# Optimization experiments

Measured on AMD Instinct MI355X. Metric: run time of the kernel, lower is better.

The kernel has to match this reference:

```python
import jax, jax.numpy as jnp
import numpy as np

B, N = 128, 1369
DINO, CLIP, H = 384, 512, 8
D = CLIP // H  # head_dim = 64
EPS = 1e-5


def setup_inputs() -> dict:
    key = jax.random.key(0)
    ks = jax.random.split(key, 8)
    s_clip = 1.0 / np.sqrt(CLIP)
    s_dino = 1.0 / np.sqrt(DINO)
    return {
        "dino_features": jax.random.normal(ks[0], (B, N, DINO), jnp.float32),
        "clip_features": jax.random.normal(ks[1], (B, CLIP), jnp.float32),
        "Wq": jax.random.uniform(ks[2], (CLIP, CLIP), jnp.float32, -s_clip, s_clip),
        "bq": jnp.zeros((CLIP,), jnp.float32),
        "Wk": jax.random.uniform(ks[3], (DINO, CLIP), jnp.float32, -s_dino, s_dino),
        "bk": jnp.zeros((CLIP,), jnp.float32),
        "Wv": jax.random.uniform(ks[4], (DINO, CLIP), jnp.float32, -s_dino, s_dino),
        "bv": jnp.zeros((CLIP,), jnp.float32),
        "temperature": jnp.ones((1,), jnp.float32),
        "ln_gamma": jnp.ones((CLIP,), jnp.float32),
        "ln_beta": jnp.zeros((CLIP,), jnp.float32),
    }


def reference(dino_features, clip_features, Wq, bq, Wk, bk, Wv, bv,
              temperature, ln_gamma, ln_beta):
    # Q: (B, H, D) -- single query token from CLIP
    Q = (clip_features @ Wq + bq).reshape(B, H, D)
    # K, V: (B, N, H, D)
    K = (dino_features @ Wk + bk).reshape(B, N, H, D)
    V = (dino_features @ Wv + bv).reshape(B, N, H, D)
    scale = jnp.sqrt(jnp.float32(D)) * temperature[0]
    # attention logits over patches: (B, H, N)
    logits = jnp.einsum("bhd,bnhd->bhn", Q, K) / scale
    attn = jax.nn.softmax(logits, axis=-1)  # dropout is identity in eval mode
    out = jnp.einsum("bhn,bnhd->bhd", attn, V).reshape(B, CLIP)
    # LayerNorm over last dim
    mu = out.mean(axis=-1, keepdims=True)
    var = out.var(axis=-1, keepdims=True)
    return (out - mu) * jax.lax.rsqrt(var + EPS) * ln_gamma + ln_beta
```

## Files before the change

kernel.cpp:

```cpp
#include <hip/hip_runtime.h>
#include <math.h>

#define B_    128
#define N_    1369
#define DINO_ 384
#define CLIP_ 512
#define H_    8
#define CHUNKS 6
#define CH     229
#define SMP    52

__device__ __forceinline__ float wave_sum(float v) {
  v += __shfl_xor(v, 1);  v += __shfl_xor(v, 2);  v += __shfl_xor(v, 4);
  v += __shfl_xor(v, 8);  v += __shfl_xor(v, 16); v += __shfl_xor(v, 32);
  return v;
}

__global__ __launch_bounds__(256) void kq(const float* __restrict__ clip,
                                          const float* __restrict__ Wq,
                                          const float* __restrict__ bq,
                                          float* __restrict__ Q) {
  const int b = blockIdx.x;
  const int c = blockIdx.y * 256 + threadIdx.x;
  __shared__ float cl[CLIP_];
  cl[threadIdx.x] = clip[b * CLIP_ + threadIdx.x];
  cl[threadIdx.x + 256] = clip[b * CLIP_ + threadIdx.x + 256];
  __syncthreads();
  float acc = bq[c];
  #pragma unroll 8
  for (int j = 0; j < CLIP_; ++j) acc += cl[j] * Wq[j * CLIP_ + c];
  Q[b * CLIP_ + c] = acc;
}

__global__ __launch_bounds__(256) void kqk(const float* __restrict__ Wk,
                                           const float* __restrict__ Q,
                                           const float* __restrict__ temp,
                                           float* __restrict__ qkout) {
  const int b = blockIdx.x;
  const int e = blockIdx.y * 256 + threadIdx.x;
  __shared__ float qs[CLIP_];
  qs[threadIdx.x] = Q[b * CLIP_ + threadIdx.x];
  qs[threadIdx.x + 256] = Q[b * CLIP_ + threadIdx.x + 256];
  __syncthreads();
  const int h = e / DINO_;
  const int j = e - h * DINO_;
  const float rs = 1.0f / (8.0f * temp[0]);
  const float* wrow = Wk + (size_t)j * CLIP_ + h * 64;
  const float* qrow = qs + h * 64;
  float a0 = 0.f, a1 = 0.f, a2 = 0.f, a3 = 0.f;
  #pragma unroll
  for (int d = 0; d < 64; d += 4) {
    const float4 wv = *(const float4*)(wrow + d);
    const float4 qv = *(const float4*)(qrow + d);
    a0 += wv.x * qv.x;  a1 += wv.y * qv.y;
    a2 += wv.z * qv.z;  a3 += wv.w * qv.w;
  }
  qkout[(size_t)b * 3072 + e] = ((a0 + a1) + (a2 + a3)) * rs;
}

__global__ __launch_bounds__(256, 3) void kmain(const float* __restrict__ dino,
                                                const float* __restrict__ qk,
                                                float* __restrict__ ps,
                                                float* __restrict__ pl) {
  const int blk = blockIdx.x;
  const int b = blk / CHUNKS;
  const int c = blk - b * CHUNKS;
  const int n0 = c * CH;
  const int n1 = min(N_, n0 + CH);
  const int tid = threadIdx.x, w = tid >> 6, lane = tid & 63;
  const int h = lane >> 3, sl = lane & 7;
  const int off = 4 * sl;

  float qr[48];
  {
    const float* qb = qk + (size_t)b * 3072 + h * DINO_ + off;
    #pragma unroll
    for (int t = 0; t < 12; ++t) {
      const float4 v = *(const float4*)(qb + 32 * t);
      qr[4*t] = v.x; qr[4*t+1] = v.y; qr[4*t+2] = v.z; qr[4*t+3] = v.w;
    }
  }
  float s[48];
  #pragma unroll
  for (int k = 0; k < 48; ++k) s[k] = 0.0f;
  float l = 0.0f;

  const float* dbase = dino + (size_t)b * N_ * DINO_ + off;

  #pragma unroll 1
  for (int n = n0 + w; n < n1; n += 4) {
    const float* row = dbase + (size_t)n * DINO_;
    float4 x[12];
    #pragma unroll
    for (int t = 0; t < 12; ++t) x[t] = *(const float4*)(row + 32 * t);

    float a0 = 0.f, a1 = 0.f, a2 = 0.f, a3 = 0.f;
    #pragma unroll
    for (int t = 0; t < 12; ++t) {
      a0 += qr[4*t]   * x[t].x;
      a1 += qr[4*t+1] * x[t].y;
      a2 += qr[4*t+2] * x[t].z;
      a3 += qr[4*t+3] * x[t].w;
    }
    float v = (a0 + a1) + (a2 + a3);
    v += __shfl_xor(v, 1);
    v += __shfl_xor(v, 2);
    v += __shfl_xor(v, 4);
    const float p = __expf(v);
    l += p;
    #pragma unroll
    for (int t = 0; t < 12; ++t) {
      s[4*t]   += p * x[t].x;
      s[4*t+1] += p * x[t].y;
      s[4*t+2] += p * x[t].z;
      s[4*t+3] += p * x[t].w;
    }
  }

  __shared__ float sm[2][64 * SMP];
  __shared__ float lm[2][H_];
  if (w >= 2) {
    float* dst = &sm[w - 2][lane * SMP];
    #pragma unroll
    for (int t = 0; t < 12; ++t)
      *(float4*)(dst + 4 * t) = make_float4(s[4*t], s[4*t+1], s[4*t+2], s[4*t+3]);
    if (sl == 0) lm[w - 2][h] = l;
  }
  __syncthreads();
  if (w < 2) {
    const float* src = &sm[w][lane * SMP];
    #pragma unroll
    for (int t = 0; t < 12; ++t) {
      const float4 v = *(const float4*)(src + 4 * t);
      s[4*t] += v.x; s[4*t+1] += v.y; s[4*t+2] += v.z; s[4*t+3] += v.w;
    }
    l += lm[w][h];
  }
  __syncthreads();
  if (w == 1) {
    float* dst = &sm[0][lane * SMP];
    #pragma unroll
    for (int t = 0; t < 12; ++t)
      *(float4*)(dst + 4 * t) = make_float4(s[4*t], s[4*t+1], s[4*t+2], s[4*t+3]);
    if (sl == 0) lm[0][h] = l;
  }
  __syncthreads();
  if (w == 0) {
    const float* src = &sm[0][lane * SMP];
    #pragma unroll
    for (int t = 0; t < 12; ++t) {
      const float4 v = *(const float4*)(src + 4 * t);
      s[4*t] += v.x; s[4*t+1] += v.y; s[4*t+2] += v.z; s[4*t+3] += v.w;
    }
    l += lm[0][h];
    float* pso = ps + (size_t)blk * 3072 + h * DINO_ + off;
    #pragma unroll
    for (int t = 0; t < 12; ++t)
      *(float4*)(pso + 32 * t) = make_float4(s[4*t], s[4*t+1], s[4*t+2], s[4*t+3]);
    if (sl == 0) pl[blk * H_ + h] = l;
  }
}

__global__ __launch_bounds__(512) void kmf(const float* __restrict__ ps,
                                           const float* __restrict__ pl,
                                           const float* __restrict__ Wv,
                                           const float* __restrict__ bv,
                                           const float* __restrict__ gamma,
                                           const float* __restrict__ beta,
                                           float* __restrict__ out) {
  const int b = blockIdx.x, tid = threadIdx.x;
  __shared__ float sfl[3072];
  __shared__ float rL[H_];
  float a[6];
  #pragma unroll
  for (int r = 0; r < 6; ++r) {
    const int e = tid + 512 * r;
    float acc = 0.0f;
    #pragma unroll
    for (int cc = 0; cc < CHUNKS; ++cc)
      acc += ps[(size_t)(b * CHUNKS + cc) * 3072 + e];
    a[r] = acc;
  }
  if (tid < H_) {
    float L = 0.0f;
    #pragma unroll
    for (int cc = 0; cc < CHUNKS; ++cc) L += pl[(b * CHUNKS + cc) * H_ + tid];
    rL[tid] = 1.0f / L;
  }
  __syncthreads();
  #pragma unroll
  for (int r = 0; r < 6; ++r) {
    const int e = tid + 512 * r;
    sfl[e] = a[r] * rL[e / DINO_];
  }
  __syncthreads();
  const int w = tid >> 6, lane = tid & 63;
  const float* srow = sfl + (tid >> 6) * DINO_;
  float acc = bv[tid];
  #pragma unroll 8
  for (int d = 0; d < DINO_; ++d) acc += srow[d] * Wv[d * CLIP_ + tid];
  float sum = wave_sum(acc);
  float sq  = wave_sum(acc * acc);
  __shared__ float rS[8], rQ[8];
  if (lane == 0) { rS[w] = sum; rQ[w] = sq; }
  __syncthreads();
  float tot = 0.0f, totq = 0.0f;
  #pragma unroll
  for (int i = 0; i < 8; ++i) { tot += rS[i]; totq += rQ[i]; }
  const float mu = tot * (1.0f / 512.0f);
  const float var = totq * (1.0f / 512.0f) - mu * mu;
  const float rstd = rsqrtf(var + 1e-5f);
  out[(size_t)b * CLIP_ + tid] = (acc - mu) * rstd * gamma[tid] + beta[tid];
}

extern "C" void kernel_launch(void* const* d_in, const int* in_sizes, int n_in,
                              void* d_out, int out_size, void* d_ws, size_t ws_size,
                              hipStream_t stream) {
  const float* dino  = (const float*)d_in[0];
  const float* clip  = (const float*)d_in[1];
  const float* Wq    = (const float*)d_in[2];
  const float* bq    = (const float*)d_in[3];
  const float* Wk    = (const float*)d_in[4];
  const float* Wv    = (const float*)d_in[6];
  const float* bv    = (const float*)d_in[7];
  const float* temp  = (const float*)d_in[8];
  const float* gamma = (const float*)d_in[9];
  const float* beta  = (const float*)d_in[10];
  float* out = (float*)d_out;

  float* ws  = (float*)d_ws;
  float* Q   = ws;
  float* qkb = Q   + 65536;
  float* ps  = qkb + 393216;
  float* pl  = ps  + 2359296;

  kq   <<<dim3(B_, 2),  256, 0, stream>>>(clip, Wq, bq, Q);
  kqk  <<<dim3(B_, 12), 256, 0, stream>>>(Wk, Q, temp, qkb);
  kmain<<<B_ * CHUNKS,  256, 0, stream>>>(dino, qkb, ps, pl);
  kmf  <<<B_,           512, 0, stream>>>(ps, pl, Wv, bv, gamma, beta, out);
}
```

Baseline: 537.9 us.

## Double-buffer dino tiles into LDS with direct global-to-LDS loads

The main attention kernel now streams 16-row tiles of the dino features into a double-buffered LDS area using the AMD global_load_lds builtin. The next tile is prefetched while the current one is consumed. Each wave then reads its rows from LDS instead of doing per-row global loads. This targets the load latency of the long sequential row loop, which leaves the kernel well short of memory bandwidth. In exchange it uses about 48KB of LDS per block, which may limit residency. It also adds a block barrier per tile and depends on the compiler inserting correct waits for the asynchronous LDS DMA before each barrier.

```diff
diff --git a/kernel.cpp b/kernel.cpp
--- a/kernel.cpp
+++ b/kernel.cpp
@@ -1,5 +1,6 @@
 #include <hip/hip_runtime.h>
 #include <math.h>
+#include <stdint.h>
 
 #define B_    128
 #define N_    1369
@@ -9,11 +10,18 @@
 #define CHUNKS 6
 #define CH     229
 #define SMP    52
+#define TROWS  16
 
 __device__ __forceinline__ float wave_sum(float v) {
   v += __shfl_xor(v, 1);  v += __shfl_xor(v, 2);  v += __shfl_xor(v, 4);
   v += __shfl_xor(v, 8);  v += __shfl_xor(v, 16); v += __shfl_xor(v, 32);
   return v;
+}
+
+__device__ __forceinline__ void gld16(const float* g, float* lds_base) {
+  __builtin_amdgcn_global_load_lds(
+      (const __attribute__((address_space(1))) void*)g,
+      (__attribute__((address_space(3))) void*)lds_base, 16, 0, 0);
 }
 
 __global__ __launch_bounds__(256) void kq(const float* __restrict__ clip,
@@ -62,6 +70,9 @@
                                                 const float* __restrict__ qk,
                                                 float* __restrict__ ps,
                                                 float* __restrict__ pl) {
+  __shared__ float lds[2 * TROWS * DINO_];
+  __shared__ float lm[2][H_];
+
   const int blk = blockIdx.x;
   const int b = blk / CHUNKS;
   const int c = blk - b * CHUNKS;
@@ -85,42 +96,74 @@
   for (int k = 0; k < 48; ++k) s[k] = 0.0f;
   float l = 0.0f;
 
-  const float* dbase = dino + (size_t)b * N_ * DINO_ + off;
-
-  #pragma unroll 1
-  for (int n = n0 + w; n < n1; n += 4) {
-    const float* row = dbase + (size_t)n * DINO_;
-    float4 x[12];
-    #pragma unroll
-    for (int t = 0; t < 12; ++t) x[t] = *(const float4*)(row + 32 * t);
-
-    float a0 = 0.f, a1 = 0.f, a2 = 0.f, a3 = 0.f;
-    #pragma unroll
-    for (int t = 0; t < 12; ++t) {
-      a0 += qr[4*t]   * x[t].x;
-      a1 += qr[4*t+1] * x[t].y;
-      a2 += qr[4*t+2] * x[t].z;
-      a3 += qr[4*t+3] * x[t].w;
-    }
-    float v = (a0 + a1) + (a2 + a3);
-    v += __shfl_xor(v, 1);
-    v += __shfl_xor(v, 2);
-    v += __shfl_xor(v, 4);
-    const float p = __expf(v);
-    l += p;
-    #pragma unroll
-    for (int t = 0; t < 12; ++t) {
-      s[4*t]   += p * x[t].x;
-      s[4*t+1] += p * x[t].y;
-      s[4*t+2] += p * x[t].z;
-      s[4*t+3] += p * x[t].w;
-    }
-  }
-
-  __shared__ float sm[2][64 * SMP];
-  __shared__ float lm[2][H_];
+  const float* gdino = dino + (size_t)b * N_ * DINO_;
+  const float* gclamp = dino + ((size_t)B_ * N_ * DINO_ - 4);
+  const int ntiles = (n1 - n0 + TROWS - 1) / TROWS;
+
+  {
+    const float* gb = gdino + (size_t)n0 * DINO_;
+    #pragma unroll
+    for (int j = 0; j < 6; ++j) {
+      const int seg = 6 * w + j;
+      const float* g = gb + (size_t)(seg * 64 + lane) * 4;
+      if (g > gclamp) g = gclamp;
+      gld16(g, lds + seg * 256);
+    }
+  }
+  __syncthreads();
+
+  for (int t = 0; t < ntiles; ++t) {
+    float* cur = lds + ((t & 1) ? TROWS * DINO_ : 0);
+    float* nxt = lds + ((t & 1) ? 0 : TROWS * DINO_);
+    if (t + 1 < ntiles) {
+      const float* gb = gdino + (size_t)(n0 + (t + 1) * TROWS) * DINO_;
+      #pragma unroll
+      for (int j = 0; j < 6; ++j) {
+        const int seg = 6 * w + j;
+        const float* g = gb + (size_t)(seg * 64 + lane) * 4;
+        if (g > gclamp) g = gclamp;
+        gld16(g, nxt + seg * 256);
+      }
+    }
+    const int tb = n0 + t * TROWS;
+    #pragma unroll 1
+    for (int k = 0; k < 4; ++k) {
+      const int slot = w + 4 * k;
+      if (tb + slot >= n1) break;
+      const float* xr = cur + slot * DINO_ + off;
+      float4 x[12];
+      #pragma unroll
+      for (int u = 0; u < 12; ++u) x[u] = *(const float4*)(xr + 32 * u);
+
+      float a0 = 0.f, a1 = 0.f, a2 = 0.f, a3 = 0.f;
+      #pragma unroll
+      for (int u = 0; u < 12; ++u) {
+        a0 += qr[4*u]   * x[u].x;
+        a1 += qr[4*u+1] * x[u].y;
+        a2 += qr[4*u+2] * x[u].z;
+        a3 += qr[4*u+3] * x[u].w;
+      }
+      float v = (a0 + a1) + (a2 + a3);
+      v += __shfl_xor(v, 1);
+      v += __shfl_xor(v, 2);
+      v += __shfl_xor(v, 4);
+      const float p = __expf(v);
+      l += p;
+      #pragma unroll
+      for (int u = 0; u < 12; ++u) {
+        s[4*u]   += p * x[u].x;
+        s[4*u+1] += p * x[u].y;
+        s[4*u+2] += p * x[u].z;
+        s[4*u+3] += p * x[u].w;
+      }
+    }
+    __syncthreads();
+  }
+
+  float* sm0 = lds;
+  float* sm1 = lds + 64 * SMP;
   if (w >= 2) {
-    float* dst = &sm[w - 2][lane * SMP];
+    float* dst = (w == 2 ? sm0 : sm1) + lane * SMP;
     #pragma unroll
     for (int t = 0; t < 12; ++t)
       *(float4*)(dst + 4 * t) = make_float4(s[4*t], s[4*t+1], s[4*t+2], s[4*t+3]);
@@ -128,7 +171,7 @@
   }
   __syncthreads();
   if (w < 2) {
-    const float* src = &sm[w][lane * SMP];
+    const float* src = (w == 0 ? sm0 : sm1) + lane * SMP;
     #pragma unroll
     for (int t = 0; t < 12; ++t) {
       const float4 v = *(const float4*)(src + 4 * t);
@@ -138,7 +181,7 @@
   }
   __syncthreads();
   if (w == 1) {
-    float* dst = &sm[0][lane * SMP];
+    float* dst = sm0 + lane * SMP;
     #pragma unroll
     for (int t = 0; t < 12; ++t)
       *(float4*)(dst + 4 * t) = make_float4(s[4*t], s[4*t+1], s[4*t+2], s[4*t+3]);
@@ -146,7 +189,7 @@
   }
   __syncthreads();
   if (w == 0) {
-    const float* src = &sm[0][lane * SMP];
+    const float* src = sm0 + lane * SMP;
     #pragma unroll
     for (int t = 0; t < 12; ++t) {
       const float4 v = *(const float4*)(src + 4 * t);
```

New measurement: 474.3 us. -11.8%, faster.
